# Optimization experiments

Measured on AMD Instinct MI355X. Metric: run time of the kernel, lower is better.

The kernel has to match this reference:

```python
import jax, jax.numpy as jnp
import numpy as np

B = 8
N_CH = 4
SZ = (128, 128, 8)
N_PTS = 100
STD = 10.0
NT = 8
NUMEL = 10 * 28 * 28 * 8  # comp_sz(128)=((128-6)//2-4)//2=28
TESS = np.array([[32,32,4],[32,96,4],[96,32,4],[96,96,4],[32,64,4],[96,64,4],[64,32,4],[64,96,4]], dtype=np.float32)


def _grid_and_dist():
    # voxel coords in np.where order (C order over sz0,sz1,sz2)
    g = jnp.stack(jnp.meshgrid(jnp.arange(SZ[0]), jnp.arange(SZ[1]), jnp.arange(SZ[2]), indexing='ij'), axis=-1).reshape(-1, 3).astype(jnp.float32)
    d = jnp.sqrt(jnp.sum((g[:, None, :] - jnp.asarray(TESS)[None]) ** 2, axis=-1))  # [N,T]
    w = jnp.exp(-d / STD)
    return g, w / w.sum(1, keepdims=True)


def _conv3d(x, w, b):
    y = jax.lax.conv_general_dilated(x, w, (1, 1, 1), 'VALID', dimension_numbers=('NCDHW', 'OIDHW', 'NCDHW'))
    return y + b[None, :, None, None, None]


def _maxpool(x):  # MaxPool3d([2,2,1], stride=[2,2,1])
    return jax.lax.reduce_window(x, -jnp.inf, jax.lax.max, (1, 1, 2, 2, 1), (1, 1, 2, 2, 1), 'VALID')


def _rigid_t(alpha, trans, sz, center):
    c, s = jnp.cos(alpha), jnp.sin(alpha)
    z = jnp.zeros_like(alpha[..., 0]); o = jnp.ones_like(z)
    b, t = trans.shape[:2]
    X = jnp.stack([c[..., 0], -s[..., 0], z, s[..., 0], c[..., 0], z, z, z, o], -1).reshape(b, t, 3, 3)
    Y = jnp.stack([c[..., 1], z, s[..., 1], z, o, z, -s[..., 1], z, c[..., 1]], -1).reshape(b, t, 3, 3)
    Z = jnp.stack([o, z, z, z, c[..., 2], -s[..., 2], z, s[..., 2], c[..., 2]], -1).reshape(b, t, 3, 3)
    R = jnp.einsum('btmn,btnk,btks->btms', X, Y, Z)
    T = trans * sz[None, None, :] + jnp.einsum('m,btmk->btk', center, jnp.eye(3, dtype=R.dtype)[None, None] - R)
    return R, T


def _grid_sample_3d(x, grid):
    # torch F.grid_sample defaults: trilinear, zeros padding, align_corners=False
    # x: [B,C,D,H,W]; grid: [B,D,H,W,3], last dim order (x->W, y->H, z->D)
    Bc, C, D, H, W = x.shape
    ix = ((grid[..., 0] + 1) * W - 1) * 0.5
    iy = ((grid[..., 1] + 1) * H - 1) * 0.5
    iz = ((grid[..., 2] + 1) * D - 1) * 0.5

    def one(xb, izb, iyb, ixb):
        z0, y0, x0 = jnp.floor(izb), jnp.floor(iyb), jnp.floor(ixb)
        out = jnp.zeros((C,) + izb.shape, x.dtype)
        for dz in (0., 1.):
            for dy in (0., 1.):
                for dx in (0., 1.):
                    zc, yc, xc = z0 + dz, y0 + dy, x0 + dx
                    w = (1 - jnp.abs(izb - zc)) * (1 - jnp.abs(iyb - yc)) * (1 - jnp.abs(ixb - xc))
                    valid = (zc >= 0) & (zc < D) & (yc >= 0) & (yc < H) & (xc >= 0) & (xc < W)
                    zi = jnp.clip(zc, 0, D - 1).astype(jnp.int32)
                    yi = jnp.clip(yc, 0, H - 1).astype(jnp.int32)
                    xi = jnp.clip(xc, 0, W - 1).astype(jnp.int32)
                    out = out + jnp.where(valid, w, 0.)[None] * xb[:, zi, yi, xi]
        return out

    return jax.vmap(one)(x, iz, iy, ix)


def _forward(x, pos, centers, conv1_w, conv1_b, conv2_w, conv2_b, fc1_w, fc1_b, fc2_w, fc2_b):
    sz = jnp.asarray(SZ, jnp.float32)
    center = sz / 2
    gpts, distw = _grid_and_dist()  # [N,3], [N,T]
    # localization CNN + fc head
    h = jax.nn.relu(_maxpool(_conv3d(x, conv1_w, conv1_b)))
    h = jax.nn.relu(_maxpool(_conv3d(h, conv2_w, conv2_b)))
    feat = h.reshape(x.shape[0], NUMEL)
    theta = jnp.tanh(jax.nn.relu(feat @ fc1_w.T + fc1_b) @ fc2_w.T + fc2_b).reshape(x.shape[0], NT, 6)
    R, T = _rigid_t(jnp.pi * theta[..., :3], theta[..., 3:], sz, center)
    # piecewise flow: weighted sum over tessellation pieces
    flow = (jnp.einsum('lk,btks->btls', gpts, R) + T[:, :, None, :]) * distw.T[None, :, :, None]  # [B,T,N,3]
    nf = (2 * flow.sum(1) / sz[None, None, :] - 1).reshape(x.shape[0], SZ[0], SZ[1], SZ[2], 3)
    grid = nf[..., ::-1]  # [..., [2,1,0]]: reorder to (x,y,z) for grid_sample
    # faithful to `if ~self.volumetric`: ~bool is always truthy in python, so always zero channel 0
    grid = grid.at[..., 0].set(0.0)
    # per-point gather regularizer + moved points (vectorized over batch)
    gridback = grid[..., ::-1]  # back to (d0,d1,d2) order
    idx = jnp.clip(jnp.round(pos), 0, sz - 1).astype(jnp.int32)
    a = jax.vmap(lambda gb, ib: gb[ib[:, 0], ib[:, 1], ib[:, 2]])(gridback, idx)  # [B,P,3]
    moved = 2 * pos - (0.5 + 0.5 * a) * (sz - 1)
    reg = jnp.mean(jnp.linalg.norm(moved - centers[None], axis=-1), axis=1)  # diag of cdist(moved, centers)
    X_t = _grid_sample_3d(x, grid)
    return X_t, grid, reg, moved


def setup_inputs() -> dict:
    key = jax.random.key(0)
    ks = jax.random.split(key, 11)
    szm1 = jnp.asarray(SZ, jnp.float32) - 1
    return {
        'x': jax.random.normal(ks[0], (B, N_CH) + SZ, jnp.float32),
        'pos': jax.random.uniform(ks[1], (B, N_PTS, 3), jnp.float32) * szm1,
        'centers': jax.random.uniform(ks[2], (N_PTS, 3), jnp.float32) * szm1,
        'conv1_w': jax.random.normal(ks[3], (8, N_CH, 7, 7, 1), jnp.float32) * 0.05,
        'conv1_b': jax.random.normal(ks[4], (8,), jnp.float32) * 0.01,
        'conv2_w': jax.random.normal(ks[5], (10, 8, 5, 5, 1), jnp.float32) * 0.05,
        'conv2_b': jax.random.normal(ks[6], (10,), jnp.float32) * 0.01,
        'fc1_w': jax.random.normal(ks[7], (32, NUMEL), jnp.float32) * 0.005,
        'fc1_b': jax.random.normal(ks[8], (32,), jnp.float32) * 0.01,
        'fc2_w': jax.random.normal(ks[9], (6 * NT, 32), jnp.float32) * 0.01,
        'fc2_b': jax.random.normal(ks[10], (6 * NT,), jnp.float32) * 0.01,
    }


def reference(x, pos, centers, conv1_w, conv1_b, conv2_w, conv2_b, fc1_w, fc1_b, fc2_w, fc2_b):
    return _forward(x, pos, centers, conv1_w, conv1_b, conv2_w, conv2_b, fc1_w, fc1_b, fc2_w, fc2_b)
```

## Files before the change

kernel.cpp:

```cpp
#include <hip/hip_runtime.h>

#define PI_F 3.14159265358979323846f

typedef _Float16 h2t __attribute__((ext_vector_type(2)));
typedef __fp16 fp16x2 __attribute__((ext_vector_type(2)));
typedef _Float16 f16x8 __attribute__((ext_vector_type(8)));
typedef float f32x4 __attribute__((ext_vector_type(4)));
typedef unsigned int uint32;

__device__ __forceinline__ uint32 packh(float a, float b) {
    h2t h = {(_Float16)a, (_Float16)b};
    return __builtin_bit_cast(uint32, h);
}
__device__ __forceinline__ uint32 pkrtz(float a, float b) {
    fp16x2 h = __builtin_amdgcn_cvt_pkrtz(a, b);
    return __builtin_bit_cast(uint32, h);
}

__global__ void k_prep(const float* __restrict__ w1, const float* __restrict__ w2,
                       uint32* __restrict__ wt1m, uint32* __restrict__ wt2m) {
    const int tid = threadIdx.x;
    for (int i = tid; i < 1792; i += 256) {
        const int idx4 = i >> 2, rem = i & 3;
        const int h = rem >> 1, icp = rem & 1;
        const int oc = idx4 & 15, kc = idx4 >> 4;
        const int ks = kc >> 2, c = kc & 3;
        const int tap = 8 * ks + c + 4 * h;
        uint32 v = 0;
        if (tap < 49 && oc < 8)
            v = packh(w1[(oc * 4 + 2 * icp) * 49 + tap],
                      w1[(oc * 4 + 2 * icp + 1) * 49 + tap]);
        wt1m[i] = v;
    }
    for (int i = tid; i < 1792; i += 256) {
        const int idx4 = i >> 2, d = i & 3;
        const int oc = idx4 & 15, kc = idx4 >> 4;
        const int ks = kc >> 2, c = kc & 3;
        const int tap = 4 * ks + c;
        uint32 v = 0;
        if (tap < 25 && oc < 10)
            v = packh(w2[(oc * 8 + 2 * d) * 25 + tap],
                      w2[(oc * 8 + 2 * d + 1) * 25 + tap]);
        wt2m[i] = v;
    }
}

__global__ __launch_bounds__(256) void k_conv1(const float* __restrict__ x,
                                               const uint32* __restrict__ wt1m,
                                               const float* __restrict__ b1,
                                               float* __restrict__ h1) {
    const int b = blockIdx.y;
    const int ty = blockIdx.x >> 4, tx = blockIdx.x & 15;
    const int py0 = ty * 4, px0 = tx * 4;
    const int iy0 = py0 * 2, ix0 = px0 * 2;

    __shared__ uint32 tin[14 * 15 * 16];

    const int tid = threadIdx.x;

    const float* xb = x + (size_t)b * 4 * 131072;
    for (int s = tid; s < 392; s += 256) {
        const int r = s / 28, rem = s % 28, c = rem >> 1, wqs = rem & 1;
        const int row = min(iy0 + r, 127), col = min(ix0 + c, 127);
        const float* base = xb + ((size_t)row * 128 + col) * 8 + wqs * 4;
        const float4 f0 = *reinterpret_cast<const float4*>(base);
        const float4 f1 = *reinterpret_cast<const float4*>(base + 131072);
        const float4 f2 = *reinterpret_cast<const float4*>(base + 262144);
        const float4 f3 = *reinterpret_cast<const float4*>(base + 393216);
        const int pos = r * 15 + c;
        const int sw = pos & 7;
        const int bi = pos * 16;
        *reinterpret_cast<uint2*>(&tin[bi + (((wqs * 4 + 0) ^ sw) << 1)]) =
            make_uint2(pkrtz(f0.x, f1.x), pkrtz(f2.x, f3.x));
        *reinterpret_cast<uint2*>(&tin[bi + (((wqs * 4 + 1) ^ sw) << 1)]) =
            make_uint2(pkrtz(f0.y, f1.y), pkrtz(f2.y, f3.y));
        *reinterpret_cast<uint2*>(&tin[bi + (((wqs * 4 + 2) ^ sw) << 1)]) =
            make_uint2(pkrtz(f0.z, f1.z), pkrtz(f2.z, f3.z));
        *reinterpret_cast<uint2*>(&tin[bi + (((wqs * 4 + 3) ^ sw) << 1)]) =
            make_uint2(pkrtz(f0.w, f1.w), pkrtz(f2.w, f3.w));
    }

    const int lane = tid & 63;
    const int wv   = tid >> 6;
    const int kc   = lane >> 4;
    const int arow = lane & 15;
    const int q    = arow >> 2, cp = arow & 3;
    const int cpy  = cp >> 1,  cpx = cp & 1;

    f16x8 Bf[7];
#pragma unroll
    for (int ks = 0; ks < 7; ++ks) {
        const uint4 t = *reinterpret_cast<const uint4*>(wt1m + (ks * 64 + lane) * 4);
        Bf[ks] = __builtin_bit_cast(f16x8, t);
    }

    int offp[7][2], sw1[7][2];
#pragma unroll
    for (int ks = 0; ks < 7; ++ks) {
#pragma unroll
        for (int h = 0; h < 2; ++h) {
            int tap = 8 * ks + kc + 4 * h;
            if (tap > 48) tap = 48;
            const int kd = tap / 7, kh = tap % 7;
            const int pos = (2 * wv + cpy + kd) * 15 + (2 * q + cpx + kh);
            offp[ks][h] = pos * 16;
            sw1[ks][h]  = pos & 7;
        }
    }

    __syncthreads();

    f32x4 acc[8];
#pragma unroll
    for (int w = 0; w < 8; ++w) acc[w] = (f32x4)(0.f);

#pragma unroll
    for (int w = 0; w < 8; ++w) {
#pragma unroll
        for (int ks = 0; ks < 7; ++ks) {
            const uint2 lo = *reinterpret_cast<const uint2*>(
                &tin[offp[ks][0] + (((w ^ sw1[ks][0])) << 1)]);
            const uint2 hi = *reinterpret_cast<const uint2*>(
                &tin[offp[ks][1] + (((w ^ sw1[ks][1])) << 1)]);
            const uint4 a4 = make_uint4(lo.x, lo.y, hi.x, hi.y);
            acc[w] = __builtin_amdgcn_mfma_f32_16x16x32_f16(
                __builtin_bit_cast(f16x8, a4), Bf[ks], acc[w], 0, 0, 0);
        }
    }

    const int oc = lane & 15, qo = lane >> 4;
    const int pi = py0 + wv, pjg = px0 + qo;
    if (oc < 8 && pi < 61 && pjg < 61) {
        const float bb = b1[oc];
        float vals[8];
#pragma unroll
        for (int w = 0; w < 8; ++w) {
            const float m = fmaxf(fmaxf(acc[w][0], acc[w][1]), fmaxf(acc[w][2], acc[w][3]));
            vals[w] = fmaxf(m + bb, 0.f);
        }
        float* base = h1 + ((((size_t)b * 8 + oc) * 61 + pi) * 61 + pjg) * 8;
        *reinterpret_cast<float4*>(base)     = make_float4(vals[0], vals[1], vals[2], vals[3]);
        *reinterpret_cast<float4*>(base + 4) = make_float4(vals[4], vals[5], vals[6], vals[7]);
    }
}

__global__ __launch_bounds__(256) void k_conv2(const float* __restrict__ h1,
                                               const uint32* __restrict__ wt2m,
                                               const float* __restrict__ b2,
                                               float* __restrict__ h2) {
    const int b = blockIdx.y;
    const int ty = blockIdx.x / 7, tx = blockIdx.x % 7;
    const int py0 = ty * 4, px0 = tx * 4;
    const int iy0 = py0 * 2, ix0 = px0 * 2;

    __shared__ uint32 tin[12 * 12 * 32];

    const int tid = threadIdx.x;

    const float* hb = h1 + (size_t)b * 8 * 29768;
    for (int s = tid; s < 288; s += 256) {
        const int pos = s >> 1, wqs = s & 1;
        const int r = pos / 12, c = pos % 12;
        const float* base = hb + ((size_t)(iy0 + r) * 61 + ix0 + c) * 8 + wqs * 4;
        const float4 f0 = *reinterpret_cast<const float4*>(base);
        const float4 f1 = *reinterpret_cast<const float4*>(base + 29768);
        const float4 f2 = *reinterpret_cast<const float4*>(base + 2 * 29768);
        const float4 f3 = *reinterpret_cast<const float4*>(base + 3 * 29768);
        const float4 f4 = *reinterpret_cast<const float4*>(base + 4 * 29768);
        const float4 f5 = *reinterpret_cast<const float4*>(base + 5 * 29768);
        const float4 f6 = *reinterpret_cast<const float4*>(base + 6 * 29768);
        const float4 f7 = *reinterpret_cast<const float4*>(base + 7 * 29768);
        const int sw = pos & 7;
        const int bi = pos * 32;
        *reinterpret_cast<uint4*>(&tin[bi + (((wqs * 4 + 0) ^ sw) << 2)]) =
            make_uint4(pkrtz(f0.x, f1.x), pkrtz(f2.x, f3.x), pkrtz(f4.x, f5.x), pkrtz(f6.x, f7.x));
        *reinterpret_cast<uint4*>(&tin[bi + (((wqs * 4 + 1) ^ sw) << 2)]) =
            make_uint4(pkrtz(f0.y, f1.y), pkrtz(f2.y, f3.y), pkrtz(f4.y, f5.y), pkrtz(f6.y, f7.y));
        *reinterpret_cast<uint4*>(&tin[bi + (((wqs * 4 + 2) ^ sw) << 2)]) =
            make_uint4(pkrtz(f0.z, f1.z), pkrtz(f2.z, f3.z), pkrtz(f4.z, f5.z), pkrtz(f6.z, f7.z));
        *reinterpret_cast<uint4*>(&tin[bi + (((wqs * 4 + 3) ^ sw) << 2)]) =
            make_uint4(pkrtz(f0.w, f1.w), pkrtz(f2.w, f3.w), pkrtz(f4.w, f5.w), pkrtz(f6.w, f7.w));
    }

    const int lane = tid & 63;
    const int wv   = tid >> 6;
    const int kc   = lane >> 4;
    const int arow = lane & 15;
    const int q    = arow >> 2, cp = arow & 3;
    const int cpy  = cp >> 1,  cpx = cp & 1;

    f16x8 Bf[7];
#pragma unroll
    for (int ks = 0; ks < 7; ++ks) {
        const uint4 t = *reinterpret_cast<const uint4*>(wt2m + (ks * 64 + lane) * 4);
        Bf[ks] = __builtin_bit_cast(f16x8, t);
    }

    int offp[7], sw2[7];
#pragma unroll
    for (int ks = 0; ks < 7; ++ks) {
        int tap = 4 * ks + kc;
        if (tap > 24) tap = 24;
        const int kd = tap / 5, kh = tap % 5;
        const int pos = (2 * wv + cpy + kd) * 12 + (2 * q + cpx + kh);
        offp[ks] = pos * 32;
        sw2[ks]  = pos & 7;
    }

    __syncthreads();

    f32x4 acc[8];
#pragma unroll
    for (int w = 0; w < 8; ++w) acc[w] = (f32x4)(0.f);

#pragma unroll
    for (int w = 0; w < 8; ++w) {
#pragma unroll
        for (int ks = 0; ks < 7; ++ks) {
            const uint4 a4 = *reinterpret_cast<const uint4*>(
                &tin[offp[ks] + (((w ^ sw2[ks])) << 2)]);
            acc[w] = __builtin_amdgcn_mfma_f32_16x16x32_f16(
                __builtin_bit_cast(f16x8, a4), Bf[ks], acc[w], 0, 0, 0);
        }
    }

    const int oc = lane & 15, qo = lane >> 4;
    const int pi = py0 + wv, pjg = px0 + qo;
    if (oc < 10) {
        const float bb = b2[oc];
        float vals[8];
#pragma unroll
        for (int w = 0; w < 8; ++w) {
            const float m = fmaxf(fmaxf(acc[w][0], acc[w][1]), fmaxf(acc[w][2], acc[w][3]));
            vals[w] = fmaxf(m + bb, 0.f);
        }
        float* base = h2 + ((((size_t)b * 10 + oc) * 28 + pi) * 28 + pjg) * 8;
        *reinterpret_cast<float4*>(base)     = make_float4(vals[0], vals[1], vals[2], vals[3]);
        *reinterpret_cast<float4*>(base + 4) = make_float4(vals[4], vals[5], vals[6], vals[7]);
    }
}

__global__ __launch_bounds__(256) void k_fc1(const float* __restrict__ feat,
                                             const float* __restrict__ w,
                                             float* __restrict__ partials) {
    const int j = blockIdx.x >> 4;
    const int kc = blockIdx.x & 15;
    const int k0 = kc * 3920;
    const float4* w4 = reinterpret_cast<const float4*>(w + (size_t)j * 62720 + k0);
    float acc[8];
#pragma unroll
    for (int b = 0; b < 8; ++b) acc[b] = 0.f;
    for (int i = threadIdx.x; i < 980; i += 256) {
        const float4 wv = w4[i];
#pragma unroll
        for (int b = 0; b < 8; ++b) {
            const float4 fv = *reinterpret_cast<const float4*>(feat + (size_t)b * 62720 + k0 + i * 4);
            acc[b] = fmaf(wv.x, fv.x, fmaf(wv.y, fv.y, fmaf(wv.z, fv.z, fmaf(wv.w, fv.w, acc[b]))));
        }
    }
#pragma unroll
    for (int b = 0; b < 8; ++b)
#pragma unroll
        for (int off = 32; off > 0; off >>= 1) acc[b] += __shfl_down(acc[b], off);
    __shared__ float red[4][8];
    const int wave = threadIdx.x >> 6;
    if ((threadIdx.x & 63) == 0)
#pragma unroll
        for (int b = 0; b < 8; ++b) red[wave][b] = acc[b];
    __syncthreads();
    if (threadIdx.x < 8) {
        partials[(j * 16 + kc) * 8 + threadIdx.x] =
            red[0][threadIdx.x] + red[1][threadIdx.x] + red[2][threadIdx.x] + red[3][threadIdx.x];
    }
}

__global__ __launch_bounds__(256) void k_flow_all(const float* __restrict__ x,
                                                  const float* __restrict__ partials,
                                                  const float* __restrict__ f1b,
                                                  const float* __restrict__ f2w,
                                                  const float* __restrict__ f2b,
                                                  const float* __restrict__ pos,
                                                  const float* __restrict__ centers,
                                                  float* __restrict__ outXt,
                                                  float* __restrict__ outGrid,
                                                  float* __restrict__ movedOut,
                                                  float* __restrict__ regOut) {
    const int b = blockIdx.y;
    const int tid = threadIdx.x;
    const int l = blockIdx.x * 256 + tid;

    __shared__ float sfo[32];
    __shared__ float srt[64];
    __shared__ float sg[768];
    __shared__ float red[128];

    if (tid < 32) {
        float s = 0.f;
#pragma unroll
        for (int kc = 0; kc < 16; ++kc) s += partials[(tid * 16 + kc) * 8 + b];
        sfo[tid] = fmaxf(s + f1b[tid], 0.f);
    }
    __syncthreads();
    if (tid < 8) {
        const int t = tid;
        float th[6];
#pragma unroll
        for (int i = 0; i < 6; ++i) {
            const int o = t * 6 + i;
            float s = f2b[o];
            const float* wr = f2w + o * 32;
#pragma unroll
            for (int k = 0; k < 32; ++k) s = fmaf(sfo[k], wr[k], s);
            th[i] = tanhf(s);
        }
        float s0, c0, s1, c1, s2, c2;
        sincosf(PI_F * th[0], &s0, &c0);
        sincosf(PI_F * th[1], &s1, &c1);
        sincosf(PI_F * th[2], &s2, &c2);
        const float R00 = c0 * c1, R10 = s0 * c1, R20 = -s1;
        const float R01 = -s0 * c2 + c0 * s1 * s2;
        const float R11 =  c0 * c2 + s0 * s1 * s2;
        const float R21 =  c1 * s2;
        const float T0 = th[3] * 128.f + 64.f - (64.f * R00 + 64.f * R10 + 4.f * R20);
        const float T1 = th[4] * 128.f + 64.f - (64.f * R01 + 64.f * R11 + 4.f * R21);
        float* o = srt + t * 8;
        o[0] = R00; o[1] = R10; o[2] = R20; o[3] = T0;
        o[4] = R01; o[5] = R11; o[6] = R21; o[7] = T1;
    }
    __syncthreads();

    const float gi = (float)(l >> 10);
    const float gj = (float)((l >> 3) & 127);
    const float gk = (float)(l & 7);

    const float tsx[8] = {32.f, 32.f, 96.f, 96.f, 32.f, 96.f, 64.f, 64.f};
    const float tsy[8] = {32.f, 96.f, 32.f, 96.f, 64.f, 64.f, 32.f, 96.f};

    float u0 = 0.f, u1 = 0.f, es = 0.f;
#pragma unroll
    for (int t = 0; t < 8; ++t) {
        float dx = gi - tsx[t], dy = gj - tsy[t], dz = gk - 4.f;
        float d = sqrtf(dx * dx + dy * dy + dz * dz);
        float e = expf(-d / 10.f);
        const float4 ra = *reinterpret_cast<const float4*>(&srt[t * 8]);
        const float4 rb = *reinterpret_cast<const float4*>(&srt[t * 8 + 4]);
        float f0 = fmaf(gi, ra.x, fmaf(gj, ra.y, fmaf(gk, ra.z, ra.w)));
        float f1 = fmaf(gi, rb.x, fmaf(gj, rb.y, fmaf(gk, rb.z, rb.w)));
        u0 = fmaf(e, f0, u0);
        u1 = fmaf(e, f1, u1);
        es += e;
    }
    const float inv = 1.f / es;
    const float fs0 = u0 * inv, fs1 = u1 * inv;
    const float nf0 = fs0 * (1.f / 64.f) - 1.f;
    const float nf1 = fs1 * (1.f / 64.f) - 1.f;

    sg[tid * 3 + 0] = 0.f;
    sg[tid * 3 + 1] = nf1;
    sg[tid * 3 + 2] = nf0;
    __syncthreads();
    if (tid < 192) {
        *reinterpret_cast<float4*>(outGrid + (size_t)b * 393216 + (size_t)blockIdx.x * 768 +
                                   tid * 4) = *reinterpret_cast<float4*>(&sg[tid * 4]);
    }

    const float iz = fs0 - 0.5f, iy = fs1 - 0.5f;
    const float z0f = floorf(iz), y0f = floorf(iy);
    const float fz = iz - z0f, fy = iy - y0f;
    const int z0 = (int)z0f, y0 = (int)y0f;
    float s0 = 0.f, s1 = 0.f, s2 = 0.f, s3 = 0.f;
    const float* xb = x + (size_t)b * 4 * 131072;
#pragma unroll
    for (int dz = 0; dz < 2; ++dz) {
        const int zc = z0 + dz;
        if (zc < 0 || zc > 127) continue;
        const float wz = dz ? fz : 1.f - fz;
#pragma unroll
        for (int dy = 0; dy < 2; ++dy) {
            const int yc = y0 + dy;
            if (yc < 0 || yc > 127) continue;
            const float wv = wz * (dy ? fy : 1.f - fy) * 0.5f;
            const float* p = xb + ((size_t)zc * 128 + yc) * 8 + 3;
            s0 = fmaf(wv, p[0] + p[1], s0);
            s1 = fmaf(wv, p[131072] + p[131073], s1);
            s2 = fmaf(wv, p[262144] + p[262145], s2);
            s3 = fmaf(wv, p[393216] + p[393217], s3);
        }
    }
    float* o = outXt + (size_t)b * 4 * 131072 + l;
    o[0] = s0; o[131072] = s1; o[262144] = s2; o[393216] = s3;

    if (blockIdx.x == 0) {
        float nrm = 0.f;
        if (tid < 128) {
            const int p = tid;
            if (p < 100) {
                const float* pp = pos + ((size_t)b * 100 + p) * 3;
                const float p0 = pp[0], p1 = pp[1], p2 = pp[2];
                int i0 = (int)rintf(p0); i0 = i0 < 0 ? 0 : (i0 > 127 ? 127 : i0);
                int i1 = (int)rintf(p1); i1 = i1 < 0 ? 0 : (i1 > 127 ? 127 : i1);
                int i2 = (int)rintf(p2); i2 = i2 < 0 ? 0 : (i2 > 7 ? 7 : i2);
                const float qi = (float)i0, qj = (float)i1, qk = (float)i2;
                float v0 = 0.f, v1 = 0.f, esm = 0.f;
#pragma unroll
                for (int t = 0; t < 8; ++t) {
                    float dx = qi - tsx[t], dy = qj - tsy[t], dz = qk - 4.f;
                    float d = sqrtf(dx * dx + dy * dy + dz * dz);
                    float e = expf(-d / 10.f);
                    const float* r = srt + t * 8;
                    float f0 = fmaf(qi, r[0], fmaf(qj, r[1], fmaf(qk, r[2], r[3])));
                    float f1 = fmaf(qi, r[4], fmaf(qj, r[5], fmaf(qk, r[6], r[7])));
                    v0 = fmaf(e, f0, v0);
                    v1 = fmaf(e, f1, v1);
                    esm += e;
                }
                const float invm = 1.f / esm;
                const float m0 = 2.f * p0 - (0.5f + 0.5f * ((v0 * invm) * (1.f / 64.f) - 1.f)) * 127.f;
                const float m1 = 2.f * p1 - (0.5f + 0.5f * ((v1 * invm) * (1.f / 64.f) - 1.f)) * 127.f;
                const float m2 = 2.f * p2 - 3.5f;
                float* mo = movedOut + ((size_t)b * 100 + p) * 3;
                mo[0] = m0; mo[1] = m1; mo[2] = m2;
                const float* ce = centers + p * 3;
                const float d0 = m0 - ce[0], d1 = m1 - ce[1], d2 = m2 - ce[2];
                nrm = sqrtf(d0 * d0 + d1 * d1 + d2 * d2);
            }
            red[tid] = nrm;
        }
        __syncthreads();
        for (int s = 64; s > 0; s >>= 1) {
            if (tid < s) red[tid] += red[tid + s];
            __syncthreads();
        }
        if (tid == 0) regOut[b] = red[0] * 0.01f;
    }
}

extern "C" void kernel_launch(void* const* d_in, const int* in_sizes, int n_in,
                              void* d_out, int out_size, void* d_ws, size_t ws_size,
                              hipStream_t stream) {
    const float* x       = (const float*)d_in[0];
    const float* pos     = (const float*)d_in[1];
    const float* centers = (const float*)d_in[2];
    const float* c1w     = (const float*)d_in[3];
    const float* c1b     = (const float*)d_in[4];
    const float* c2w     = (const float*)d_in[5];
    const float* c2b     = (const float*)d_in[6];
    const float* f1w     = (const float*)d_in[7];
    const float* f1b     = (const float*)d_in[8];
    const float* f2w     = (const float*)d_in[9];
    const float* f2b     = (const float*)d_in[10];

    float* out = (float*)d_out;
    float* ws  = (float*)d_ws;

    float* h1       = ws;
    float* h2       = h1 + 1905152;
    float* partials = h2 + 501760;

    float* outXt    = out;
    float* outGrid  = out + 4194304;
    float* outReg   = out + 4194304 + 3145728;
    float* outMoved = outReg + 8;

    uint32* wt1m = (uint32*)(out + 4194304 + 3145728 - 4096);
    uint32* wt2m = wt1m + 1792;

    k_prep<<<1, 256, 0, stream>>>(c1w, c2w, wt1m, wt2m);
    k_conv1<<<dim3(256, 8), 256, 0, stream>>>(x, wt1m, c1b, h1);
    k_conv2<<<dim3(49, 8), 256, 0, stream>>>(h1, wt2m, c2b, h2);
    k_fc1<<<512, 256, 0, stream>>>(h2, f1w, partials);
    k_flow_all<<<dim3(512, 8), 256, 0, stream>>>(x, partials, f1b, f2w, f2b, pos, centers,
                                                 outXt, outGrid, outMoved, outReg);
}
```

Measured before the change: 67.85 us.

## Fold weight packing into conv kernels and restructure fc1 reduction

Drops the separate weight-prep launch: each conv block now packs its own fp16 MFMA weight fragments into shared memory, then loads them into registers after the barrier. The fc1 kernel is rewritten to use 160 blocks that stage a slice of features for all batches in shared memory. Each thread computes one (output, batch) dot product over that slice, with no shuffle or shared reductions. The flow kernel now sums 160 partials per output instead of 16. This saves one launch and the reduction overhead, at the cost of redundant weight packing in every conv block, more shared memory per block, and a longer serial partial sum.

```diff
diff --git a/kernel.cpp b/kernel.cpp
--- a/kernel.cpp
+++ b/kernel.cpp
@@ -17,36 +17,8 @@
     return __builtin_bit_cast(uint32, h);
 }
 
-__global__ void k_prep(const float* __restrict__ w1, const float* __restrict__ w2,
-                       uint32* __restrict__ wt1m, uint32* __restrict__ wt2m) {
-    const int tid = threadIdx.x;
-    for (int i = tid; i < 1792; i += 256) {
-        const int idx4 = i >> 2, rem = i & 3;
-        const int h = rem >> 1, icp = rem & 1;
-        const int oc = idx4 & 15, kc = idx4 >> 4;
-        const int ks = kc >> 2, c = kc & 3;
-        const int tap = 8 * ks + c + 4 * h;
-        uint32 v = 0;
-        if (tap < 49 && oc < 8)
-            v = packh(w1[(oc * 4 + 2 * icp) * 49 + tap],
-                      w1[(oc * 4 + 2 * icp + 1) * 49 + tap]);
-        wt1m[i] = v;
-    }
-    for (int i = tid; i < 1792; i += 256) {
-        const int idx4 = i >> 2, d = i & 3;
-        const int oc = idx4 & 15, kc = idx4 >> 4;
-        const int ks = kc >> 2, c = kc & 3;
-        const int tap = 4 * ks + c;
-        uint32 v = 0;
-        if (tap < 25 && oc < 10)
-            v = packh(w2[(oc * 8 + 2 * d) * 25 + tap],
-                      w2[(oc * 8 + 2 * d + 1) * 25 + tap]);
-        wt2m[i] = v;
-    }
-}
-
 __global__ __launch_bounds__(256) void k_conv1(const float* __restrict__ x,
-                                               const uint32* __restrict__ wt1m,
+                                               const float* __restrict__ w1,
                                                const float* __restrict__ b1,
                                                float* __restrict__ h1) {
     const int b = blockIdx.y;
@@ -55,8 +27,22 @@
     const int iy0 = py0 * 2, ix0 = px0 * 2;
 
     __shared__ uint32 tin[14 * 15 * 16];
+    __shared__ uint32 wl[1792];
 
     const int tid = threadIdx.x;
+
+    for (int i = tid; i < 1792; i += 256) {
+        const int idx4 = i >> 2, rem = i & 3;
+        const int h = rem >> 1, icp = rem & 1;
+        const int oc = idx4 & 15, kcg = idx4 >> 4;
+        const int ks = kcg >> 2, c = kcg & 3;
+        const int tap = 8 * ks + c + 4 * h;
+        uint32 v = 0;
+        if (tap < 49 && oc < 8)
+            v = packh(w1[(oc * 4 + 2 * icp) * 49 + tap],
+                      w1[(oc * 4 + 2 * icp + 1) * 49 + tap]);
+        wl[i] = v;
+    }
 
     const float* xb = x + (size_t)b * 4 * 131072;
     for (int s = tid; s < 392; s += 256) {
@@ -87,13 +73,6 @@
     const int q    = arow >> 2, cp = arow & 3;
     const int cpy  = cp >> 1,  cpx = cp & 1;
 
-    f16x8 Bf[7];
-#pragma unroll
-    for (int ks = 0; ks < 7; ++ks) {
-        const uint4 t = *reinterpret_cast<const uint4*>(wt1m + (ks * 64 + lane) * 4);
-        Bf[ks] = __builtin_bit_cast(f16x8, t);
-    }
-
     int offp[7][2], sw1[7][2];
 #pragma unroll
     for (int ks = 0; ks < 7; ++ks) {
@@ -109,6 +88,13 @@
     }
 
     __syncthreads();
+
+    f16x8 Bf[7];
+#pragma unroll
+    for (int ks = 0; ks < 7; ++ks) {
+        const uint4 t = *reinterpret_cast<const uint4*>(&wl[(ks * 64 + lane) * 4]);
+        Bf[ks] = __builtin_bit_cast(f16x8, t);
+    }
 
     f32x4 acc[8];
 #pragma unroll
@@ -145,7 +131,7 @@
 }
 
 __global__ __launch_bounds__(256) void k_conv2(const float* __restrict__ h1,
-                                               const uint32* __restrict__ wt2m,
+                                               const float* __restrict__ w2,
                                                const float* __restrict__ b2,
                                                float* __restrict__ h2) {
     const int b = blockIdx.y;
@@ -154,8 +140,21 @@
     const int iy0 = py0 * 2, ix0 = px0 * 2;
 
     __shared__ uint32 tin[12 * 12 * 32];
+    __shared__ uint32 wl[1792];
 
     const int tid = threadIdx.x;
+
+    for (int i = tid; i < 1792; i += 256) {
+        const int idx4 = i >> 2, d = i & 3;
+        const int oc = idx4 & 15, kcg = idx4 >> 4;
+        const int ks = kcg >> 2, c = kcg & 3;
+        const int tap = 4 * ks + c;
+        uint32 v = 0;
+        if (tap < 25 && oc < 10)
+            v = packh(w2[(oc * 8 + 2 * d) * 25 + tap],
+                      w2[(oc * 8 + 2 * d + 1) * 25 + tap]);
+        wl[i] = v;
+    }
 
     const float* hb = h1 + (size_t)b * 8 * 29768;
     for (int s = tid; s < 288; s += 256) {
@@ -189,13 +188,6 @@
     const int q    = arow >> 2, cp = arow & 3;
     const int cpy  = cp >> 1,  cpx = cp & 1;
 
-    f16x8 Bf[7];
-#pragma unroll
-    for (int ks = 0; ks < 7; ++ks) {
-        const uint4 t = *reinterpret_cast<const uint4*>(wt2m + (ks * 64 + lane) * 4);
-        Bf[ks] = __builtin_bit_cast(f16x8, t);
-    }
-
     int offp[7], sw2[7];
 #pragma unroll
     for (int ks = 0; ks < 7; ++ks) {
@@ -209,6 +201,13 @@
 
     __syncthreads();
 
+    f16x8 Bf[7];
+#pragma unroll
+    for (int ks = 0; ks < 7; ++ks) {
+        const uint4 t = *reinterpret_cast<const uint4*>(&wl[(ks * 64 + lane) * 4]);
+        Bf[ks] = __builtin_bit_cast(f16x8, t);
+    }
+
     f32x4 acc[8];
 #pragma unroll
     for (int w = 0; w < 8; ++w) acc[w] = (f32x4)(0.f);
@@ -243,35 +242,30 @@
 __global__ __launch_bounds__(256) void k_fc1(const float* __restrict__ feat,
                                              const float* __restrict__ w,
                                              float* __restrict__ partials) {
-    const int j = blockIdx.x >> 4;
-    const int kc = blockIdx.x & 15;
-    const int k0 = kc * 3920;
-    const float4* w4 = reinterpret_cast<const float4*>(w + (size_t)j * 62720 + k0);
-    float acc[8];
-#pragma unroll
-    for (int b = 0; b < 8; ++b) acc[b] = 0.f;
-    for (int i = threadIdx.x; i < 980; i += 256) {
-        const float4 wv = w4[i];
-#pragma unroll
-        for (int b = 0; b < 8; ++b) {
-            const float4 fv = *reinterpret_cast<const float4*>(feat + (size_t)b * 62720 + k0 + i * 4);
-            acc[b] = fmaf(wv.x, fv.x, fmaf(wv.y, fv.y, fmaf(wv.z, fv.z, fmaf(wv.w, fv.w, acc[b]))));
-        }
-    }
-#pragma unroll
-    for (int b = 0; b < 8; ++b)
-#pragma unroll
-        for (int off = 32; off > 0; off >>= 1) acc[b] += __shfl_down(acc[b], off);
-    __shared__ float red[4][8];
-    const int wave = threadIdx.x >> 6;
-    if ((threadIdx.x & 63) == 0)
-#pragma unroll
-        for (int b = 0; b < 8; ++b) red[wave][b] = acc[b];
-    __syncthreads();
-    if (threadIdx.x < 8) {
-        partials[(j * 16 + kc) * 8 + threadIdx.x] =
-            red[0][threadIdx.x] + red[1][threadIdx.x] + red[2][threadIdx.x] + red[3][threadIdx.x];
-    }
+    const int blk = blockIdx.x;
+    const int tid = threadIdx.x;
+
+    __shared__ float sf[8 * 392];
+
+    const float4* f4g = reinterpret_cast<const float4*>(feat);
+    for (int s = tid; s < 784; s += 256) {
+        const int b = s / 98, i = s % 98;
+        *reinterpret_cast<float4*>(&sf[(b * 98 + i) * 4]) =
+            f4g[(size_t)b * 15680 + blk * 98 + i];
+    }
+    __syncthreads();
+
+    const int j = tid >> 3, b = tid & 7;
+    const float4* wp = reinterpret_cast<const float4*>(w) + (size_t)j * 15680 + blk * 98;
+    const float4* fp = reinterpret_cast<const float4*>(&sf[b * 392]);
+    float acc = 0.f;
+#pragma unroll 7
+    for (int i = 0; i < 98; ++i) {
+        const float4 wv = wp[i];
+        const float4 fv = fp[i];
+        acc = fmaf(wv.x, fv.x, fmaf(wv.y, fv.y, fmaf(wv.z, fv.z, fmaf(wv.w, fv.w, acc))));
+    }
+    partials[(j * 160 + blk) * 8 + b] = acc;
 }
 
 __global__ __launch_bounds__(256) void k_flow_all(const float* __restrict__ x,
@@ -296,8 +290,7 @@
 
     if (tid < 32) {
         float s = 0.f;
-#pragma unroll
-        for (int kc = 0; kc < 16; ++kc) s += partials[(tid * 16 + kc) * 8 + b];
+        for (int kc = 0; kc < 160; ++kc) s += partials[(tid * 160 + kc) * 8 + b];
         sfo[tid] = fmaxf(s + f1b[tid], 0.f);
     }
     __syncthreads();
@@ -462,13 +455,9 @@
     float* outReg   = out + 4194304 + 3145728;
     float* outMoved = outReg + 8;
 
-    uint32* wt1m = (uint32*)(out + 4194304 + 3145728 - 4096);
-    uint32* wt2m = wt1m + 1792;
-
-    k_prep<<<1, 256, 0, stream>>>(c1w, c2w, wt1m, wt2m);
-    k_conv1<<<dim3(256, 8), 256, 0, stream>>>(x, wt1m, c1b, h1);
-    k_conv2<<<dim3(49, 8), 256, 0, stream>>>(h1, wt2m, c2b, h2);
-    k_fc1<<<512, 256, 0, stream>>>(h2, f1w, partials);
+    k_conv1<<<dim3(256, 8), 256, 0, stream>>>(x, c1w, c1b, h1);
+    k_conv2<<<dim3(49, 8), 256, 0, stream>>>(h1, c2w, c2b, h2);
+    k_fc1<<<160, 256, 0, stream>>>(h2, f1w, partials);
     k_flow_all<<<dim3(512, 8), 256, 0, stream>>>(x, partials, f1b, f2w, f2b, pos, centers,
                                                  outXt, outGrid, outMoved, outReg);
 }
```

Measured after the change: 103.9 us. +53.2%, slower.
